# Optimization experiments

Hardware: AMD Instinct MI355X
Metric: run time of the kernel (lower is better)

Reference implementation:

```python
import jax, jax.numpy as jnp
import numpy as np

# Module constants (from init_kwargs)
SR = 16000
HOP_LENGTH = 256
HOP_MS = 40
WIN_LENGTHS = (80, 160)
MARGIN = 0.2
SPOOF_WEIGHT = 0.5
MEL_SAMPLE = 16
MAX_TIME_WINDOWS = 64
SEED = 123
EPS = 1e-12  # F.normalize default eps


def _ms_to_frames(ms):
    samples = int(SR * (ms / 1000.0))
    return max(3, samples // HOP_LENGTH)


def _window_starts(T, w_frames, hop_frames):
    # Replicates _frames() + linspace capping (all static, done in numpy).
    starts = np.arange(0, T - w_frames + 1, hop_frames, dtype=np.int64)
    if starts.size == 0:
        return np.zeros((1,), dtype=np.int64), T
    if MAX_TIME_WINDOWS and starts.size > MAX_TIME_WINDOWS:
        sel = np.linspace(0, starts.size - 1, MAX_TIME_WINDOWS).astype(np.int64)
        starts = starts[sel]
    return starts, w_frames


def _mel_indices(M):
    if MEL_SAMPLE and MEL_SAMPLE < M:
        return np.random.default_rng(SEED).permutation(M)[:MEL_SAMPLE]
    return np.arange(M)


def _head(x, W1, W2):
    # 1x1 convs (no bias) == per-pixel channel GEMMs.  x: [B,C,M,T]
    h = jax.nn.relu(jnp.einsum('bcmt,oc->bomt', x, W1))
    return jnp.einsum('bcmt,oc->bomt', h, W2)


def _cosine_distance(u, v):
    un = u / jnp.maximum(jnp.linalg.norm(u, axis=-1, keepdims=True), EPS)
    vn = v / jnp.maximum(jnp.linalg.norm(v, axis=-1, keepdims=True), EPS)
    return 1.0 - (un * vn).sum(axis=-1)


def _windowed_dists(A_sel, P_sel, starts, w):
    # A_sel, P_sel: [B, C, Ms, T]; gather all windows at once.
    B, C, Ms, T = A_sel.shape
    nW = starts.shape[0]
    idx = jnp.asarray(starts[:, None] + np.arange(w)[None, :]).ravel()  # [nW*w]
    u = jnp.take(A_sel, idx, axis=3).reshape(B, C, Ms, nW, w)
    v = jnp.take(P_sel, idx, axis=3).reshape(B, C, Ms, nW, w)
    # flatten (C, w) per window -> feature dim (dot/norm are order-invariant)
    u = jnp.moveaxis(u, 1, 3).reshape(B, Ms, nW, C * w)
    v = jnp.moveaxis(v, 1, 3).reshape(B, Ms, nW, C * w)
    return _cosine_distance(u, v).reshape(B, Ms * nW)  # [B, Ms*nW]


def _forward(A_map, P_map, y, W1a, W2a, W1p, W2p):
    B, _, M, T = A_map.shape
    A_loc = _head(A_map, W1a, W2a)
    P_loc = _head(P_map, W1p, W2p)
    idx_m = _mel_indices(M)
    A_sel = A_loc[:, :, idx_m, :]
    P_sel = P_loc[:, :, idx_m, :]
    hop_frames = _ms_to_frames(HOP_MS)

    dists = []
    for w_ms in WIN_LENGTHS:
        w = _ms_to_frames(w_ms)
        starts, w_eff = _window_starts(T, w, hop_frames)
        dists.append(_windowed_dists(A_sel, P_sel, starts, w_eff))
    D = jnp.concatenate(dists, axis=1)  # [B, n_total_windows]

    mask_r = (y == 0)
    mask_s = (y == 1)
    nr = mask_r.sum()
    ns = mask_s.sum()
    mr = mask_r.astype(D.dtype)
    ms_ = mask_s.astype(D.dtype)
    # per-window mean over real samples, then mean over windows (== sum/count)
    real_mean = (D * mr[:, None]).sum(axis=0) / jnp.maximum(nr, 1).astype(D.dtype)
    spoof_mean = (jax.nn.relu(MARGIN - D) * ms_[:, None]).sum(axis=0) / jnp.maximum(ns, 1).astype(D.dtype)
    loss_real = jnp.where(nr > 0, real_mean.mean(), jnp.array(0.0, D.dtype))
    loss_spoof = jnp.where(ns > 0, spoof_mean.mean(), jnp.array(0.0, D.dtype))
    stc_loss = loss_real + SPOOF_WEIGHT * loss_spoof  # tv_weight = 0
    coh_score = 1.0 - D.mean(axis=1)  # [B]
    return stc_loss, coh_score


def setup_inputs() -> dict:
    key = jax.random.key(0)
    k = jax.random.split(key, 8)
    B, M, T = 32, 80, 2000
    return {
        'A_map': jax.random.normal(k[0], (B, 1, M, T), dtype=jnp.float32),
        'P_map': jax.random.normal(k[1], (B, 1, M, T), dtype=jnp.float32),
        'y': jax.random.randint(k[2], (B,), 0, 2, dtype=jnp.int32),
        'W1a': jax.random.normal(k[3], (8, 1), dtype=jnp.float32) * 0.5,
        'W2a': jax.random.normal(k[4], (8, 8), dtype=jnp.float32) * 0.25,
        'W1p': jax.random.normal(k[5], (8, 1), dtype=jnp.float32) * 0.5,
        'W2p': jax.random.normal(k[6], (8, 8), dtype=jnp.float32) * 0.25,
    }


def reference(A_map, P_map, y, W1a, W2a, W1p, W2p):
    return _forward(A_map, P_map, y, W1a, W2a, W1p, W2p)
```

## Files before the change

### kernel.cpp

```cpp
#include <hip/hip_runtime.h>
#include <stdint.h>

#define NB 32
#define NM 80
#define NT 2000
#define MSEL 16
#define NWIN 128
#define NBLK (NB * MSEL)
#define NCOLS 2048.0f

struct Params {
    int mel[MSEL];
    int start[NWIN];
};

__global__ __launch_bounds__(128) void asn_win_kernel(
    const float* __restrict__ A, const float* __restrict__ P,
    const float* __restrict__ W1a, const float* __restrict__ W2a,
    const float* __restrict__ W1p, const float* __restrict__ W2p,
    float* __restrict__ ws, Params prm)
{
    __shared__ float4 sA4[NT / 4];
    __shared__ float4 sP4[NT / 4];
    __shared__ float sK[4];
    __shared__ float sSA[2];
    __shared__ float sSP[2];
    __shared__ float wsum[2][2];

    float* sA = (float*)sA4;
    float* sP = (float*)sP4;

    const int blk = blockIdx.x;
    const int b   = blk >> 4;
    const int msi = blk & 15;
    const int m   = prm.mel[msi];
    const int tid = threadIdx.x;

    if (tid == 0) {
        float cap[8], can[8], cqp[8], cqn[8];
        #pragma unroll
        for (int o = 0; o < 8; ++o) { cap[o]=0.f; can[o]=0.f; cqp[o]=0.f; cqn[o]=0.f; }
        #pragma unroll
        for (int c = 0; c < 8; ++c) {
            float wa = W1a[c], wp = W1p[c];
            #pragma unroll
            for (int o = 0; o < 8; ++o) {
                float ta = wa * W2a[o * 8 + c];
                float tp = wp * W2p[o * 8 + c];
                if (wa > 0.f) cap[o] += ta; else if (wa < 0.f) can[o] += ta;
                if (wp > 0.f) cqp[o] += tp; else if (wp < 0.f) cqn[o] += tp;
            }
        }
        float kpp=0.f,kpn=0.f,knp=0.f,knn=0.f,sap=0.f,san=0.f,spp=0.f,spn=0.f;
        #pragma unroll
        for (int o = 0; o < 8; ++o) {
            kpp += cap[o]*cqp[o];  kpn += cap[o]*cqn[o];
            knp += can[o]*cqp[o];  knn += can[o]*cqn[o];
            sap += cap[o]*cap[o];  san += can[o]*can[o];
            spp += cqp[o]*cqp[o];  spn += cqn[o]*cqn[o];
        }
        sK[3]=kpp; sK[2]=kpn; sK[1]=knp; sK[0]=knn;
        sSA[1]=sap; sSA[0]=san;
        sSP[1]=spp; sSP[0]=spn;
    }

    const float4* arow = (const float4*)(A + ((size_t)b * NM + m) * NT);
    const float4* prow = (const float4*)(P + ((size_t)b * NM + m) * NT);
    for (int t = tid; t < NT / 4; t += 128) {
        sA4[t] = arow[t];
        sP4[t] = prow[t];
    }
    __syncthreads();

    const int w = (tid < 64) ? 5 : 10;
    const int s = prm.start[tid];
    float dot = 0.f, na = 0.f, npv = 0.f;
    for (int t = 0; t < w; ++t) {
        float a = sA[s + t];
        float p = sP[s + t];
        int ia = (a >= 0.f) ? 1 : 0;
        int ip = (p >= 0.f) ? 1 : 0;
        dot += a * p * sK[ia * 2 + ip];
        na  += a * a * sSA[ia];
        npv += p * p * sSP[ip];
    }
    float nu = fmaxf(sqrtf(na),  1e-12f);
    float nv = fmaxf(sqrtf(npv), 1e-12f);
    float dist = 1.f - dot / (nu * nv);
    float rd   = fmaxf(0.2f - dist, 0.f);

    float s1 = dist, s2 = rd;
    for (int off = 32; off; off >>= 1) {
        s1 += __shfl_down(s1, off);
        s2 += __shfl_down(s2, off);
    }
    if ((tid & 63) == 0) {
        wsum[tid >> 6][0] = s1;
        wsum[tid >> 6][1] = s2;
    }
    __syncthreads();
    if (tid == 0) {
        ws[2 * blk]     = wsum[0][0] + wsum[1][0];
        ws[2 * blk + 1] = wsum[0][1] + wsum[1][1];
    }
}

__global__ __launch_bounds__(64) void asn_final_kernel(
    const float* __restrict__ ws, const int* __restrict__ y,
    float* __restrict__ out)
{
    const int tid = threadIdx.x;

    float aR = 0.f, aS = 0.f;
    float colsum[8];
    #pragma unroll
    for (int r = 0; r < 8; ++r) {
        int k  = r * 64 + tid;
        int bb = k >> 4;
        float d  = ws[2 * k];
        float sv = ws[2 * k + 1];
        if (y[bb] == 0) aR += d; else aS += sv;
        colsum[r] = d;
    }
    #pragma unroll
    for (int off = 32; off; off >>= 1) {
        aR += __shfl_down(aR, off);
        aS += __shfl_down(aS, off);
    }

    #pragma unroll
    for (int r = 0; r < 8; ++r) {
        float v = colsum[r];
        #pragma unroll
        for (int off = 8; off; off >>= 1) v += __shfl_down(v, off);
        if ((tid & 15) == 0) {
            int bb = r * 4 + (tid >> 4);
            out[1 + bb] = 1.f - v * (1.0f / NCOLS);
        }
    }

    if (tid == 0) {
        int nr = 0, ns = 0;
        for (int bb = 0; bb < NB; ++bb) { int yb = y[bb]; nr += (yb == 0); ns += (yb == 1); }
        float lr = aR / (NCOLS * (float)(nr > 0 ? nr : 1));
        float ls = aS / (NCOLS * (float)(ns > 0 ? ns : 1));
        out[0] = lr + 0.5f * ls;
    }
}

static void compute_params(Params& prm)
{
    const uint32_t INIT_A = 0x43b0d7e5u, MULT_A = 0x931e8875u;
    const uint32_t INIT_B = 0x8b51f9ddu, MULT_B = 0x58f38dedu;

    uint32_t hc = INIT_A;
    auto hashmix = [&](uint32_t v) -> uint32_t {
        v ^= hc; hc *= MULT_A; v *= hc; v ^= v >> 16; return v;
    };
    auto mix = [](uint32_t x, uint32_t y) -> uint32_t {
        uint32_t r = (x * 0xca01f9ddu) ^ (y * 0x4973f715u);
        r ^= r >> 16; return r;
    };

    uint32_t pool[4];
    const uint32_t entropy[1] = { 123u };
    for (int i = 0; i < 4; ++i) pool[i] = hashmix(i < 1 ? entropy[i] : 0u);
    for (int s = 0; s < 4; ++s)
        for (int d = 0; d < 4; ++d)
            if (s != d) pool[d] = mix(pool[d], hashmix(pool[s]));

    uint32_t w32[8];
    uint32_t hc2 = INIT_B;
    for (int i = 0; i < 8; ++i) {
        uint32_t v = pool[i & 3];
        v ^= hc2; hc2 *= MULT_B; v *= hc2; v ^= v >> 16;
        w32[i] = v;
    }
    uint64_t sd[4];
    for (int i = 0; i < 4; ++i)
        sd[i] = (uint64_t)w32[2 * i] | ((uint64_t)w32[2 * i + 1] << 32);

    typedef __uint128_t u128;
    const u128 MULT = ((u128)0x2360ed051fc65da4ULL << 64) | 0x4385df649fccf645ULL;
    u128 initstate = ((u128)sd[0] << 64) | sd[1];
    u128 initseq   = ((u128)sd[2] << 64) | sd[3];
    u128 state = 0, inc = (initseq << 1) | 1;
    state = state * MULT + inc;
    state += initstate;
    state = state * MULT + inc;

    bool has32 = false; uint32_t buf32 = 0;
    auto next64 = [&]() -> uint64_t {
        state = state * MULT + inc;
        uint64_t hi = (uint64_t)(state >> 64);
        uint64_t lo = (uint64_t)state;
        uint64_t x = hi ^ lo;
        unsigned rot = (unsigned)(state >> 122);
        return (x >> rot) | (x << ((64u - rot) & 63u));
    };
    auto next32 = [&]() -> uint32_t {
        if (has32) { has32 = false; return buf32; }
        uint64_t v = next64();
        has32 = true; buf32 = (uint32_t)(v >> 32);
        return (uint32_t)v;
    };

    int perm[NM];
    for (int i = 0; i < NM; ++i) perm[i] = i;
    for (int i = NM - 1; i >= 1; --i) {
        uint32_t mask = (uint32_t)i;
        mask |= mask >> 1; mask |= mask >> 2; mask |= mask >> 4;
        mask |= mask >> 8; mask |= mask >> 16;
        uint32_t j;
        do { j = next32() & mask; } while (j > (uint32_t)i);
        int tmp = perm[i]; perm[i] = perm[(int)j]; perm[(int)j] = tmp;
    }
    for (int i = 0; i < MSEL; ++i) prm.mel[i] = perm[i];

    {
        const double step = 665.0 / 63.0;
        for (int i = 0; i < 64; ++i) {
            long long sel = (i == 63) ? 665LL : (long long)((double)i * step);
            prm.start[i] = (int)(3LL * sel);
        }
    }
    {
        const double step = 663.0 / 63.0;
        for (int i = 0; i < 64; ++i) {
            long long sel = (i == 63) ? 663LL : (long long)((double)i * step);
            prm.start[64 + i] = (int)(3LL * sel);
        }
    }
}

extern "C" void kernel_launch(void* const* d_in, const int* in_sizes, int n_in,
                              void* d_out, int out_size, void* d_ws, size_t ws_size,
                              hipStream_t stream)
{
    const float* A   = (const float*)d_in[0];
    const float* P   = (const float*)d_in[1];
    const int*   y   = (const int*)d_in[2];
    const float* W1a = (const float*)d_in[3];
    const float* W2a = (const float*)d_in[4];
    const float* W1p = (const float*)d_in[5];
    const float* W2p = (const float*)d_in[6];
    float* out = (float*)d_out;
    float* ws  = (float*)d_ws;

    Params prm;
    compute_params(prm);

    asn_win_kernel<<<dim3(NBLK), dim3(128), 0, stream>>>(
        A, P, W1a, W2a, W1p, W2p, ws, prm);
    asn_final_kernel<<<dim3(1), dim3(64), 0, stream>>>(ws, y, out);
}
```

Before: 99.89 us.

## Fuse final reduction into window kernel via last-block atomic counter

Merges the two-kernel pipeline into one launch: each block writes its partial sums to a device global array and increments an atomic counter, and the last block to finish performs the final loss and coherence reduction. The window loop is also templated on the window length so it can be fully unrolled. This removes a kernel launch and the gap between dependent kernels. The cost is a threadfence and atomic per block, plus a modulo-wrapped counter that must stay in sync across calls.

New measurement: 106.2 us. +6.3%, slower.

```diff
diff --git a/kernel.cpp b/kernel.cpp
--- a/kernel.cpp
+++ b/kernel.cpp
@@ -14,11 +14,33 @@
     int start[NWIN];
 };
 
-__global__ __launch_bounds__(128) void asn_win_kernel(
+__device__ float2   g_part[NBLK];
+__device__ unsigned g_cnt = 0;
+
+template <int W>
+__device__ inline void win_acc(const float* __restrict__ sA,
+                               const float* __restrict__ sP,
+                               int s, const float* sK, const float* sSA,
+                               const float* sSP,
+                               float& dot, float& na, float& npv)
+{
+    #pragma unroll
+    for (int t = 0; t < W; ++t) {
+        float a = sA[s + t];
+        float p = sP[s + t];
+        int ia = (a >= 0.f) ? 1 : 0;
+        int ip = (p >= 0.f) ? 1 : 0;
+        dot += a * p * sK[ia * 2 + ip];
+        na  += a * a * sSA[ia];
+        npv += p * p * sSP[ip];
+    }
+}
+
+__global__ __launch_bounds__(128) void asn_fused_kernel(
     const float* __restrict__ A, const float* __restrict__ P,
     const float* __restrict__ W1a, const float* __restrict__ W2a,
     const float* __restrict__ W1p, const float* __restrict__ W2p,
-    float* __restrict__ ws, Params prm)
+    const int* __restrict__ y, float* __restrict__ out, Params prm)
 {
     __shared__ float4 sA4[NT / 4];
     __shared__ float4 sP4[NT / 4];
@@ -26,6 +48,7 @@
     __shared__ float sSA[2];
     __shared__ float sSP[2];
     __shared__ float wsum[2][2];
+    __shared__ int   s_last;
 
     float* sA = (float*)sA4;
     float* sP = (float*)sP4;
@@ -72,24 +95,18 @@
     }
     __syncthreads();
 
-    const int w = (tid < 64) ? 5 : 10;
     const int s = prm.start[tid];
     float dot = 0.f, na = 0.f, npv = 0.f;
-    for (int t = 0; t < w; ++t) {
-        float a = sA[s + t];
-        float p = sP[s + t];
-        int ia = (a >= 0.f) ? 1 : 0;
-        int ip = (p >= 0.f) ? 1 : 0;
-        dot += a * p * sK[ia * 2 + ip];
-        na  += a * a * sSA[ia];
-        npv += p * p * sSP[ip];
-    }
+    if (tid < 64) win_acc<5> (sA, sP, s, sK, sSA, sSP, dot, na, npv);
+    else          win_acc<10>(sA, sP, s, sK, sSA, sSP, dot, na, npv);
+
     float nu = fmaxf(sqrtf(na),  1e-12f);
     float nv = fmaxf(sqrtf(npv), 1e-12f);
     float dist = 1.f - dot / (nu * nv);
     float rd   = fmaxf(0.2f - dist, 0.f);
 
     float s1 = dist, s2 = rd;
+    #pragma unroll
     for (int off = 32; off; off >>= 1) {
         s1 += __shfl_down(s1, off);
         s2 += __shfl_down(s2, off);
@@ -99,51 +116,53 @@
         wsum[tid >> 6][1] = s2;
     }
     __syncthreads();
+
     if (tid == 0) {
-        ws[2 * blk]     = wsum[0][0] + wsum[1][0];
-        ws[2 * blk + 1] = wsum[0][1] + wsum[1][1];
-    }
-}
-
-__global__ __launch_bounds__(64) void asn_final_kernel(
-    const float* __restrict__ ws, const int* __restrict__ y,
-    float* __restrict__ out)
-{
-    const int tid = threadIdx.x;
-
+        float2 v = make_float2(wsum[0][0] + wsum[1][0],
+                               wsum[0][1] + wsum[1][1]);
+        g_part[blk] = v;
+        __threadfence();
+        unsigned old = atomicAdd(&g_cnt, 1u);
+        s_last = ((old & (NBLK - 1)) == (NBLK - 1)) ? 1 : 0;
+    }
+    __syncthreads();
+    if (!s_last) return;
+
+    __threadfence();
+
+    float* sD = sA;
     float aR = 0.f, aS = 0.f;
-    float colsum[8];
-    #pragma unroll
-    for (int r = 0; r < 8; ++r) {
-        int k  = r * 64 + tid;
-        int bb = k >> 4;
-        float d  = ws[2 * k];
-        float sv = ws[2 * k + 1];
-        if (y[bb] == 0) aR += d; else aS += sv;
-        colsum[r] = d;
+    #pragma unroll
+    for (int r = 0; r < 4; ++r) {
+        int k = r * 128 + tid;
+        float2 v = g_part[k];
+        sD[k] = v.x;
+        if (y[k >> 4] == 0) aR += v.x; else aS += v.y;
     }
     #pragma unroll
     for (int off = 32; off; off >>= 1) {
         aR += __shfl_down(aR, off);
         aS += __shfl_down(aS, off);
     }
-
-    #pragma unroll
-    for (int r = 0; r < 8; ++r) {
-        float v = colsum[r];
-        #pragma unroll
-        for (int off = 8; off; off >>= 1) v += __shfl_down(v, off);
-        if ((tid & 15) == 0) {
-            int bb = r * 4 + (tid >> 4);
-            out[1 + bb] = 1.f - v * (1.0f / NCOLS);
-        }
-    }
-
+    if ((tid & 63) == 0) {
+        wsum[tid >> 6][0] = aR;
+        wsum[tid >> 6][1] = aS;
+    }
+    __syncthreads();
+
+    if (tid < NB) {
+        float v = 0.f;
+        #pragma unroll
+        for (int i = 0; i < 16; ++i) v += sD[tid * 16 + i];
+        out[1 + tid] = 1.f - v * (1.0f / NCOLS);
+    }
     if (tid == 0) {
         int nr = 0, ns = 0;
         for (int bb = 0; bb < NB; ++bb) { int yb = y[bb]; nr += (yb == 0); ns += (yb == 1); }
-        float lr = aR / (NCOLS * (float)(nr > 0 ? nr : 1));
-        float ls = aS / (NCOLS * (float)(ns > 0 ? ns : 1));
+        float aRt = wsum[0][0] + wsum[1][0];
+        float aSt = wsum[0][1] + wsum[1][1];
+        float lr = aRt / (NCOLS * (float)(nr > 0 ? nr : 1));
+        float ls = aSt / (NCOLS * (float)(ns > 0 ? ns : 1));
         out[0] = lr + 0.5f * ls;
     }
 }
@@ -173,7 +192,7 @@
     uint32_t hc2 = INIT_B;
     for (int i = 0; i < 8; ++i) {
         uint32_t v = pool[i & 3];
-        v ^= hc2; hc2 *= MULT_B; v *= hc2; v ^= v >> 16;
+        v ^= hc2; hc2 *= MULT_B; v ^= 0u; v *= hc2; v ^= v >> 16;
         w32[i] = v;
     }
     uint64_t sd[4];
@@ -245,12 +264,11 @@
     const float* W1p = (const float*)d_in[5];
     const float* W2p = (const float*)d_in[6];
     float* out = (float*)d_out;
-    float* ws  = (float*)d_ws;
+    (void)d_ws; (void)ws_size;
 
     Params prm;
     compute_params(prm);
 
-    asn_win_kernel<<<dim3(NBLK), dim3(128), 0, stream>>>(
-        A, P, W1a, W2a, W1p, W2p, ws, prm);
-    asn_final_kernel<<<dim3(1), dim3(64), 0, stream>>>(ws, y, out);
-}
+    asn_fused_kernel<<<dim3(NBLK), dim3(128), 0, stream>>>(
+        A, P, W1a, W2a, W1p, W2p, y, out, prm);
+}
```
